# Optimization experiments

Measured on AMD Instinct MI355X. Metric: run time of the kernel, lower is better.

Reference implementation:

```python
import jax, jax.numpy as jnp
import numpy as np

B, T, C = 4, 2048, 1024
H = 16
D = C // H  # 64


def setup_inputs() -> dict:
    key = jax.random.key(0)
    k1, k2, k3 = jax.random.split(key, 3)
    x = jax.random.normal(k1, (B, T, C), dtype=jnp.float32)
    W_attn = jax.random.normal(k2, (C, 3 * C), dtype=jnp.float32) * (1.0 / np.sqrt(C))
    W_proj = jax.random.normal(k3, (C, C), dtype=jnp.float32) * (1.0 / np.sqrt(C))
    return {"x": x, "W_attn": W_attn, "W_proj": W_proj}


def reference(x, W_attn, W_proj):
    b, t, c = x.shape
    # qkv projection: [B,T,3C]
    qkv = jnp.einsum('btc,cd->btd', x, W_attn)
    q, k, v = jnp.split(qkv, 3, axis=-1)
    # split heads -> [B,H,T,D]
    q = q.reshape(b, t, H, D).transpose(0, 2, 1, 3)
    k = k.reshape(b, t, H, D).transpose(0, 2, 1, 3)
    v = v.reshape(b, t, H, D).transpose(0, 2, 1, 3)
    # scores scaled by 1/sqrt(C) (faithful to source: uses full embed dim)
    att = jnp.einsum('bhtd,bhsd->bhts', q, k) * (1.0 / jnp.sqrt(jnp.float32(c)))
    # causal mask: -inf where key index > query index
    causal = jnp.tril(jnp.ones((t, t), dtype=bool))
    att = jnp.where(causal, att, jnp.float32(-jnp.inf))
    att = jax.nn.softmax(att, axis=-1)
    # attention output -> combine heads
    y = jnp.einsum('bhts,bhsd->bhtd', att, v)
    y = y.transpose(0, 2, 1, 3).reshape(b, t, c)
    z = jnp.einsum('btc,cd->btd', y, W_proj)
    return z
```

## Files before the change

### kernel.cpp

```cpp
#include <hip/hip_runtime.h>
#include <hip/hip_bf16.h>

typedef __bf16 bf16x8 __attribute__((ext_vector_type(8)));
typedef float f32x4 __attribute__((ext_vector_type(4)));

static __device__ __forceinline__ __bf16 tobf(float x) {
    __hip_bfloat16 h = __float2bfloat16(x);
    __bf16 r;
    __builtin_memcpy(&r, &h, 2);
    return r;
}

static __device__ __forceinline__ float fexp2(float x) {
    float r;
    asm("v_exp_f32 %0, %1" : "=v"(r) : "v"(x));
    return r;
}

__global__ __launch_bounds__(256) void prep_k(const float* __restrict__ x,
                                              __hip_bfloat16* __restrict__ x_bf,
                                              const float* __restrict__ Wa,
                                              __hip_bfloat16* __restrict__ WaT,
                                              const float* __restrict__ Wp,
                                              __hip_bfloat16* __restrict__ WpT) {
    __shared__ float tile[32][33];
    const int bid = blockIdx.x;
    const int tid = threadIdx.x;
    if (bid < 8192) {
        int i = bid * 256 + tid;
        float4 v = reinterpret_cast<const float4*>(x)[i];
        __hip_bfloat16 a = __float2bfloat16(v.x);
        __hip_bfloat16 b = __float2bfloat16(v.y);
        __hip_bfloat16 c = __float2bfloat16(v.z);
        __hip_bfloat16 d = __float2bfloat16(v.w);
        ushort4 o;
        o.x = *reinterpret_cast<unsigned short*>(&a);
        o.y = *reinterpret_cast<unsigned short*>(&b);
        o.z = *reinterpret_cast<unsigned short*>(&c);
        o.w = *reinterpret_cast<unsigned short*>(&d);
        reinterpret_cast<ushort4*>(x_bf)[i] = o;
        return;
    }
    const float* in;
    __hip_bfloat16* out;
    int bx, Cn, qrows;
    float qscale;
    int t;
    if (bid < 8192 + 3072) {
        t = bid - 8192;
        in = Wa; out = WaT; Cn = 3072; qrows = 1024;
        qscale = 0.045084223f;
        bx = t % 96;
    } else {
        t = bid - 11264;
        in = Wp; out = WpT; Cn = 1024; qrows = 0;
        qscale = 1.0f;
        bx = t % 32;
    }
    const int by = (bid < 11264) ? (t / 96) : (t / 32);
    const int R = 1024;
    const int c0 = bx * 32, r0 = by * 32;
    const int tx = tid & 31, ty = tid >> 5;
#pragma unroll
    for (int i = 0; i < 4; ++i)
        tile[ty + i * 8][tx] = in[(size_t)(r0 + ty + i * 8) * Cn + c0 + tx];
    __syncthreads();
#pragma unroll
    for (int i = 0; i < 4; ++i) {
        int orow = c0 + ty + i * 8;
        float v = tile[tx][ty + i * 8];
        if (orow < qrows) v *= qscale;
        out[(size_t)orow * R + r0 + tx] = __float2bfloat16(v);
    }
}

__global__ __launch_bounds__(256) void vtrans_k(const __hip_bfloat16* __restrict__ qkv,
                                                __hip_bfloat16* __restrict__ Vt) {
    __shared__ __hip_bfloat16 tile[32][33];
    const int bh = blockIdx.z, b = bh >> 4, h = bh & 15;
    const int tt = blockIdx.x;
    const int dt = blockIdx.y;
    const int tx = threadIdx.x & 31, ty = threadIdx.x >> 5;
    const __hip_bfloat16* src = qkv + (size_t)b * 2048 * 3072 + 2048 + h * 64;
#pragma unroll
    for (int i = 0; i < 4; ++i)
        tile[ty + i * 8][tx] = src[(size_t)(tt * 32 + ty + i * 8) * 3072 + dt * 32 + tx];
    __syncthreads();
    const int slot = ((tx & 12) << 1) | (tx & 3) | ((tx >> 4) << 2);
    __hip_bfloat16* dst = Vt + ((size_t)bh * 64 + dt * 32) * 2048 + tt * 32;
#pragma unroll
    for (int i = 0; i < 4; ++i)
        dst[(size_t)(ty + i * 8) * 2048 + slot] = tile[tx][ty + i * 8];
}

template <bool OUT_BF16>
__global__ __launch_bounds__(256) void gemm_bt(const __hip_bfloat16* __restrict__ A,
                                               const __hip_bfloat16* __restrict__ Bt,
                                               __hip_bfloat16* __restrict__ Cb,
                                               float* __restrict__ Cf,
                                               int M, int N, int K) {
    __shared__ __attribute__((aligned(16))) __hip_bfloat16 As[128 * 32];
    __shared__ __attribute__((aligned(16))) __hip_bfloat16 Bs[128 * 32];
    const int tid = threadIdx.x;
    const int lane = tid & 63, wid = tid >> 6;
    const int l15 = lane & 15, lg = lane >> 4;
    const int wr = wid >> 1, wc = wid & 1;
    const int lin = blockIdx.y * gridDim.x + blockIdx.x;
    const int cpx = (gridDim.x * gridDim.y) >> 3;
    const int sw = (lin & 7) * cpx + (lin >> 3);
    const int bn = sw % gridDim.x, bm = sw / gridDim.x;
    const size_t arow0 = (size_t)bm * 128;
    const size_t brow0 = (size_t)bn * 128;

    f32x4 acc[4][4] = {};

    const int nk = K >> 5;
    for (int kt = 0; kt < nk; ++kt) {
        __syncthreads();
        {
            const int k0 = kt * 32;
#pragma unroll
            for (int p = 0; p < 2; ++p) {
                int idx = p * 256 + tid;
                int row = idx >> 2;
                int cc = (idx & 3) * 8;
                const __hip_bfloat16* ga = A + (arow0 + row) * (size_t)K + k0 + cc;
                const __hip_bfloat16* gb = Bt + (brow0 + row) * (size_t)K + k0 + cc;
                __builtin_amdgcn_global_load_lds(
                    (const __attribute__((address_space(1))) void*)ga,
                    (__attribute__((address_space(3))) void*)(&As[idx * 8]), 16, 0, 0);
                __builtin_amdgcn_global_load_lds(
                    (const __attribute__((address_space(1))) void*)gb,
                    (__attribute__((address_space(3))) void*)(&Bs[idx * 8]), 16, 0, 0);
            }
        }
        __syncthreads();
        bf16x8 af[4], bfr[4];
#pragma unroll
        for (int m = 0; m < 4; ++m)
            af[m] = *reinterpret_cast<const bf16x8*>(&As[(wr * 64 + m * 16 + l15) * 32 + lg * 8]);
#pragma unroll
        for (int n = 0; n < 4; ++n)
            bfr[n] = *reinterpret_cast<const bf16x8*>(&Bs[(wc * 64 + n * 16 + l15) * 32 + lg * 8]);
#pragma unroll
        for (int m = 0; m < 4; ++m)
#pragma unroll
            for (int n = 0; n < 4; ++n)
                acc[m][n] = __builtin_amdgcn_mfma_f32_16x16x32_bf16(af[m], bfr[n], acc[m][n], 0, 0, 0);
    }

#pragma unroll
    for (int m = 0; m < 4; ++m) {
#pragma unroll
        for (int n = 0; n < 4; ++n) {
#pragma unroll
            for (int j = 0; j < 4; ++j) {
                int row = bm * 128 + wr * 64 + m * 16 + lg * 4 + j;
                int col = bn * 128 + wc * 64 + n * 16 + l15;
                if (OUT_BF16)
                    Cb[(size_t)row * N + col] = __float2bfloat16(acc[m][n][j]);
                else
                    Cf[(size_t)row * N + col] = acc[m][n][j];
            }
        }
    }
}

__global__ __launch_bounds__(128) void attn_k(const __hip_bfloat16* __restrict__ qkv,
                                              const __hip_bfloat16* __restrict__ Vt,
                                              __hip_bfloat16* __restrict__ y) {
    constexpr int TT = 2048;
    constexpr int S3C = 3072;
    const int bh = blockIdx.x, b = bh >> 4, h = bh & 15;
    const int tid = threadIdx.x;
    const int wid = tid >> 6, lane = tid & 63;
    const int l15 = lane & 15, lg = lane >> 4;

    __shared__ __attribute__((aligned(16))) char Ks[2][64 * 128];

    const __hip_bfloat16* base = qkv + (size_t)b * TT * S3C;
    const int qo = h * 64, ko = 1024 + h * 64;
    const __hip_bfloat16* vt = Vt + (size_t)bh * 64 * TT;

    bf16x8 vones;
#pragma unroll
    for (int i = 0; i < 8; ++i) vones[i] = tobf(1.0f);

#define STAGE(BUF, KT)                                                                             \
    do {                                                                                           \
        const int kb_ = (KT) * 64;                                                                 \
        _Pragma("unroll") for (int p_ = 0; p_ < 4; ++p_) {                                         \
            int idx_ = p_ * 128 + tid;                                                             \
            int row_ = idx_ >> 3, c_ = idx_ & 7;                                                   \
            int col_ = 8 * (c_ ^ (row_ & 7));                                                      \
            __builtin_amdgcn_global_load_lds(                                                      \
                (const __attribute__((address_space(1))) void*)(base + (size_t)(kb_ + row_) * S3C + ko + col_), \
                (__attribute__((address_space(3))) void*)(&Ks[BUF][idx_ * 16]), 16, 0, 0);         \
        }                                                                                          \
    } while (0)

#pragma unroll 1
    for (int pass = 0; pass < 2; ++pass) {
        const int qt = pass == 0 ? (31 - (int)blockIdx.y) : (int)blockIdx.y;
        const int qbase = qt * 64 + wid * 32;
        const int nt = qt + 1;

        bf16x8 aq[2][2];
#pragma unroll
        for (int m = 0; m < 2; ++m) {
            const __hip_bfloat16* qp = base + (size_t)(qbase + m * 16 + l15) * S3C + qo + lg * 8;
            aq[m][0] = *reinterpret_cast<const bf16x8*>(qp);
            aq[m][1] = *reinterpret_cast<const bf16x8*>(qp + 32);
        }

        f32x4 acc[2][4] = {};
        f32x4 lsum[2] = {};

        STAGE(0, 0);
        asm volatile("s_waitcnt vmcnt(0)" ::: "memory");
        __syncthreads();

        int cur = 0;
        for (int kt = 0; kt < nt; ++kt) {
            if (kt + 1 < nt) STAGE(cur ^ 1, kt + 1);
            const int kb = kt * 64;
            const char* Kb = &Ks[cur][0];
            const int sw = l15 & 7;
            f32x4 s[2][4];
            __builtin_amdgcn_s_setprio(1);
#pragma unroll
            for (int cg = 0; cg < 4; ++cg) {
                const char* krow = Kb + (cg * 16 + l15) * 128;
                bf16x8 k0 = *reinterpret_cast<const bf16x8*>(krow + 16 * (lg ^ sw));
                bf16x8 k1 = *reinterpret_cast<const bf16x8*>(krow + 16 * ((4 + lg) ^ sw));
#pragma unroll
                for (int m = 0; m < 2; ++m) {
                    f32x4 z = {0.f, 0.f, 0.f, 0.f};
                    z = __builtin_amdgcn_mfma_f32_16x16x32_bf16(k0, aq[m][0], z, 0, 0, 0);
                    z = __builtin_amdgcn_mfma_f32_16x16x32_bf16(k1, aq[m][1], z, 0, 0, 0);
                    s[m][cg] = z;
                }
            }
            __builtin_amdgcn_s_setprio(0);
            bf16x8 vb[2][4];
#pragma unroll
            for (int dg = 0; dg < 4; ++dg) {
                const __hip_bfloat16* vrow = vt + (size_t)(dg * 16 + l15) * TT + kb + lg * 8;
                vb[0][dg] = *reinterpret_cast<const bf16x8*>(vrow);
                vb[1][dg] = *reinterpret_cast<const bf16x8*>(vrow + 32);
            }
            float p[2][4][4];
            const bool needmask = (kb + 63 > qbase);
#pragma unroll
            for (int m = 0; m < 2; ++m)
#pragma unroll
                for (int cg = 0; cg < 4; ++cg)
#pragma unroll
                    for (int j = 0; j < 4; ++j) {
                        float e = fexp2(s[m][cg][j]);
                        if (needmask) {
                            int key = kb + cg * 16 + lg * 4 + j;
                            int qrow = qbase + m * 16 + l15;
                            e = (key > qrow) ? 0.f : e;
                        }
                        p[m][cg][j] = e;
                    }
            bf16x8 pa[2][2];
#pragma unroll
            for (int m = 0; m < 2; ++m)
#pragma unroll
                for (int ks = 0; ks < 2; ++ks) {
                    bf16x8 t;
                    t[0] = tobf(p[m][2 * ks][0]);
                    t[1] = tobf(p[m][2 * ks][1]);
                    t[2] = tobf(p[m][2 * ks][2]);
                    t[3] = tobf(p[m][2 * ks][3]);
                    t[4] = tobf(p[m][2 * ks + 1][0]);
                    t[5] = tobf(p[m][2 * ks + 1][1]);
                    t[6] = tobf(p[m][2 * ks + 1][2]);
                    t[7] = tobf(p[m][2 * ks + 1][3]);
                    pa[m][ks] = t;
                }
            __builtin_amdgcn_s_setprio(1);
#pragma unroll
            for (int ks = 0; ks < 2; ++ks) {
#pragma unroll
                for (int dg = 0; dg < 4; ++dg)
#pragma unroll
                    for (int m = 0; m < 2; ++m)
                        acc[m][dg] = __builtin_amdgcn_mfma_f32_16x16x32_bf16(pa[m][ks], vb[ks][dg],
                                                                             acc[m][dg], 0, 0, 0);
#pragma unroll
                for (int m = 0; m < 2; ++m)
                    lsum[m] = __builtin_amdgcn_mfma_f32_16x16x32_bf16(pa[m][ks], vones,
                                                                      lsum[m], 0, 0, 0);
            }
            __builtin_amdgcn_s_setprio(0);
            asm volatile("s_waitcnt vmcnt(0)" ::: "memory");
            __syncthreads();
            cur ^= 1;
        }

#pragma unroll
        for (int m = 0; m < 2; ++m)
#pragma unroll
            for (int j = 0; j < 4; ++j) {
                float inv = 1.f / lsum[m][j];
                int t = qbase + m * 16 + lg * 4 + j;
#pragma unroll
                for (int dg = 0; dg < 4; ++dg) {
                    float o = acc[m][dg][j] * inv;
                    y[((size_t)(b * TT + t)) * 1024 + h * 64 + dg * 16 + l15] = __float2bfloat16(o);
                }
            }
    }
#undef STAGE
}

extern "C" void kernel_launch(void* const* d_in, const int* in_sizes, int n_in,
                              void* d_out, int out_size, void* d_ws, size_t ws_size,
                              hipStream_t stream) {
    const float* x = (const float*)d_in[0];
    const float* Wa = (const float*)d_in[1];
    const float* Wp = (const float*)d_in[2];
    float* out = (float*)d_out;

    __hip_bfloat16* ws = (__hip_bfloat16*)d_ws;
    __hip_bfloat16* x_bf = ws;
    __hip_bfloat16* WaT = x_bf + (size_t)8192 * 1024;
    __hip_bfloat16* WpT = WaT + (size_t)3072 * 1024;
    __hip_bfloat16* qkv = WpT + (size_t)1024 * 1024;
    __hip_bfloat16* ybf = qkv + (size_t)8192 * 3072;
    __hip_bfloat16* Vt = x_bf;

    prep_k<<<8192 + 3072 + 1024, 256, 0, stream>>>(x, x_bf, Wa, WaT, Wp, WpT);
    gemm_bt<true><<<dim3(24, 64), 256, 0, stream>>>(x_bf, WaT, qkv, nullptr, 8192, 3072, 1024);
    vtrans_k<<<dim3(64, 2, 64), 256, 0, stream>>>(qkv, Vt);
    attn_k<<<dim3(64, 16), 128, 0, stream>>>(qkv, Vt, ybf);
    gemm_bt<false><<<dim3(8, 64), 256, 0, stream>>>(ybf, WpT, nullptr, out, 8192, 1024, 1024);
}
```

Before: 195.6 us.

## Deepen attention K/V prefetch pipeline with triple LDS buffer and register double-buffering

The attention kernel now stages K tiles two iterations ahead in a three-slot LDS ring. It also loads the next tile's K fragments and V operands into alternating register sets while the current tile computes. The end-of-iteration wait is relaxed from vmcnt(0) to vmcnt(8), so the K stage can complete while the next V register loads stay in flight, and the launch bounds add a minimum of 2 blocks per unit. The aim is to hide global and LDS latency behind MFMA work. The cost is higher register and LDS pressure, which could reduce occupancy or cause spills.

```diff
diff --git a/kernel.cpp b/kernel.cpp
--- a/kernel.cpp
+++ b/kernel.cpp
@@ -166,9 +166,9 @@
     }
 }
 
-__global__ __launch_bounds__(128) void attn_k(const __hip_bfloat16* __restrict__ qkv,
-                                              const __hip_bfloat16* __restrict__ Vt,
-                                              __hip_bfloat16* __restrict__ y) {
+__global__ __launch_bounds__(128, 2) void attn_k(const __hip_bfloat16* __restrict__ qkv,
+                                                 const __hip_bfloat16* __restrict__ Vt,
+                                                 __hip_bfloat16* __restrict__ y) {
     constexpr int TT = 2048;
     constexpr int S3C = 3072;
     const int bh = blockIdx.x, b = bh >> 4, h = bh & 15;
@@ -176,7 +176,7 @@
     const int wid = tid >> 6, lane = tid & 63;
     const int l15 = lane & 15, lg = lane >> 4;
 
-    __shared__ __attribute__((aligned(16))) char Ks[2][64 * 128];
+    __shared__ __attribute__((aligned(16))) char Ks[3][64 * 128];
 
     const __hip_bfloat16* base = qkv + (size_t)b * TT * S3C;
     const int qo = h * 64, ko = 1024 + h * 64;
@@ -204,6 +204,7 @@
         const int qt = pass == 0 ? (31 - (int)blockIdx.y) : (int)blockIdx.y;
         const int qbase = qt * 64 + wid * 32;
         const int nt = qt + 1;
+        const int sw = l15 & 7;
 
         bf16x8 aq[2][2];
 #pragma unroll
@@ -216,38 +217,64 @@
         f32x4 acc[2][4] = {};
         f32x4 lsum[2] = {};
 
+        bf16x8 kfA[4][2], kfB[4][2];
+        bf16x8 vbA[2][4], vbB[2][4];
+
         STAGE(0, 0);
+        STAGE(1, nt > 1 ? 1 : 0);
         asm volatile("s_waitcnt vmcnt(0)" ::: "memory");
         __syncthreads();
-
-        int cur = 0;
-        for (int kt = 0; kt < nt; ++kt) {
-            if (kt + 1 < nt) STAGE(cur ^ 1, kt + 1);
+        {
+            const char* Kb = &Ks[0][0];
+#pragma unroll
+            for (int cg = 0; cg < 4; ++cg) {
+                const char* krow = Kb + (cg * 16 + l15) * 128;
+                kfA[cg][0] = *reinterpret_cast<const bf16x8*>(krow + 16 * (lg ^ sw));
+                kfA[cg][1] = *reinterpret_cast<const bf16x8*>(krow + 16 * ((4 + lg) ^ sw));
+            }
+#pragma unroll
+            for (int dg = 0; dg < 4; ++dg) {
+                const __hip_bfloat16* vrow = vt + (size_t)(dg * 16 + l15) * TT + lg * 8;
+                vbA[0][dg] = *reinterpret_cast<const bf16x8*>(vrow);
+                vbA[1][dg] = *reinterpret_cast<const bf16x8*>(vrow + 32);
+            }
+        }
+
+        auto step = [&](bf16x8 (&kfc)[4][2], bf16x8 (&vbc)[2][4],
+                        bf16x8 (&kfn)[4][2], bf16x8 (&vbn)[2][4],
+                        int kt, int bnxt, int bstg) {
             const int kb = kt * 64;
-            const char* Kb = &Ks[cur][0];
-            const int sw = l15 & 7;
+            if (kt + 1 < nt) {
+                const char* Kb = &Ks[bnxt][0];
+#pragma unroll
+                for (int cg = 0; cg < 4; ++cg) {
+                    const char* krow = Kb + (cg * 16 + l15) * 128;
+                    kfn[cg][0] = *reinterpret_cast<const bf16x8*>(krow + 16 * (lg ^ sw));
+                    kfn[cg][1] = *reinterpret_cast<const bf16x8*>(krow + 16 * ((4 + lg) ^ sw));
+                }
+            }
+            if (kt + 2 < nt) STAGE(bstg, kt + 2);
+            __builtin_amdgcn_sched_barrier(0);
             f32x4 s[2][4];
             __builtin_amdgcn_s_setprio(1);
 #pragma unroll
-            for (int cg = 0; cg < 4; ++cg) {
-                const char* krow = Kb + (cg * 16 + l15) * 128;
-                bf16x8 k0 = *reinterpret_cast<const bf16x8*>(krow + 16 * (lg ^ sw));
-                bf16x8 k1 = *reinterpret_cast<const bf16x8*>(krow + 16 * ((4 + lg) ^ sw));
+            for (int cg = 0; cg < 4; ++cg)
 #pragma unroll
                 for (int m = 0; m < 2; ++m) {
                     f32x4 z = {0.f, 0.f, 0.f, 0.f};
-                    z = __builtin_amdgcn_mfma_f32_16x16x32_bf16(k0, aq[m][0], z, 0, 0, 0);
-                    z = __builtin_amdgcn_mfma_f32_16x16x32_bf16(k1, aq[m][1], z, 0, 0, 0);
+                    z = __builtin_amdgcn_mfma_f32_16x16x32_bf16(kfc[cg][0], aq[m][0], z, 0, 0, 0);
+                    z = __builtin_amdgcn_mfma_f32_16x16x32_bf16(kfc[cg][1], aq[m][1], z, 0, 0, 0);
                     s[m][cg] = z;
                 }
-            }
             __builtin_amdgcn_s_setprio(0);
-            bf16x8 vb[2][4];
-#pragma unroll
-            for (int dg = 0; dg < 4; ++dg) {
-                const __hip_bfloat16* vrow = vt + (size_t)(dg * 16 + l15) * TT + kb + lg * 8;
-                vb[0][dg] = *reinterpret_cast<const bf16x8*>(vrow);
-                vb[1][dg] = *reinterpret_cast<const bf16x8*>(vrow + 32);
+            if (kt + 1 < nt) {
+                const int kb2 = kb + 64;
+#pragma unroll
+                for (int dg = 0; dg < 4; ++dg) {
+                    const __hip_bfloat16* vrow = vt + (size_t)(dg * 16 + l15) * TT + kb2 + lg * 8;
+                    vbn[0][dg] = *reinterpret_cast<const bf16x8*>(vrow);
+                    vbn[1][dg] = *reinterpret_cast<const bf16x8*>(vrow + 32);
+                }
             }
             float p[2][4][4];
             const bool needmask = (kb + 63 > qbase);
@@ -288,7 +315,7 @@
                 for (int dg = 0; dg < 4; ++dg)
 #pragma unroll
                     for (int m = 0; m < 2; ++m)
-                        acc[m][dg] = __builtin_amdgcn_mfma_f32_16x16x32_bf16(pa[m][ks], vb[ks][dg],
+                        acc[m][dg] = __builtin_amdgcn_mfma_f32_16x16x32_bf16(pa[m][ks], vbc[ks][dg],
                                                                              acc[m][dg], 0, 0, 0);
 #pragma unroll
                 for (int m = 0; m < 2; ++m)
@@ -296,9 +323,20 @@
                                                                       lsum[m], 0, 0, 0);
             }
             __builtin_amdgcn_s_setprio(0);
-            asm volatile("s_waitcnt vmcnt(0)" ::: "memory");
+            asm volatile("s_waitcnt vmcnt(8)" ::: "memory");
             __syncthreads();
-            cur ^= 1;
+        };
+
+        int kt = 0, bcur = 0, bnxt = 1, bstg = 2;
+#pragma unroll 1
+        while (kt < nt) {
+            step(kfA, vbA, kfB, vbB, kt, bnxt, bstg);
+            { int t0 = bcur; bcur = bnxt; bnxt = bstg; bstg = t0; }
+            ++kt;
+            if (kt >= nt) break;
+            step(kfB, vbB, kfA, vbA, kt, bnxt, bstg);
+            { int t0 = bcur; bcur = bnxt; bnxt = bstg; bstg = t0; }
+            ++kt;
         }
 
 #pragma unroll
@@ -313,6 +351,8 @@
                     y[((size_t)(b * TT + t)) * 1024 + h * 64 + dg * 16 + l15] = __float2bfloat16(o);
                 }
             }
+        asm volatile("s_waitcnt vmcnt(0)" ::: "memory");
+        __syncthreads();
     }
 #undef STAGE
 }
```

Result: slower. 275.1 us (+40.6%).
